# Kernel optimization log

Measured on AMD Instinct MI355X. Metric: run time of the kernel, lower is better.

The kernel has to match this reference:

```python
import jax, jax.numpy as jnp
import numpy as np
import math

D_MODEL = 1024
N_HEADS = 16
HEAD_DIM = D_MODEL // N_HEADS
RANK = 128
SCALE = 1.0 / math.sqrt(HEAD_DIM)


def lowrank(x, u, v, b):
    # y = (x @ u) @ v + b : d_model -> rank -> d_model
    return jnp.einsum('bsd,dr,re->bse', x, u, v) + b


def setup_inputs() -> dict:
    key = jax.random.key(0)
    ks = jax.random.split(key, 16)
    B, S = 2, 2048
    inp = {
        'q': jax.random.normal(ks[0], (B, S, D_MODEL), jnp.float32),
        'k': jax.random.normal(ks[1], (B, S, D_MODEL), jnp.float32),
        'v': jax.random.normal(ks[2], (B, S, D_MODEL), jnp.float32),
        'mask': jnp.ones((B, S), jnp.int32),
    }
    i = 3
    for name in ('q', 'k', 'v', 'out'):
        inp[f'{name}_u'] = jax.random.normal(ks[i], (D_MODEL, RANK), jnp.float32) * 0.02
        inp[f'{name}_v'] = jax.random.normal(ks[i + 1], (RANK, D_MODEL), jnp.float32) * 0.02
        inp[f'{name}_b'] = jnp.zeros((D_MODEL,), jnp.float32)
        i += 2
    return inp


def reference(q, k, v, mask, q_u, q_v, q_b, k_u, k_v, k_b, v_u, v_v, v_b, out_u, out_v, out_b):
    B, S, _ = q.shape
    qh = lowrank(q, q_u, q_v, q_b).reshape(B, S, N_HEADS, HEAD_DIM)
    kh = lowrank(k, k_u, k_v, k_b).reshape(B, S, N_HEADS, HEAD_DIM)
    vh = lowrank(v, v_u, v_v, v_b).reshape(B, S, N_HEADS, HEAD_DIM)
    # scores: [B, H, Sq, Sk]
    scores = jnp.einsum('bqhd,bkhd->bhqk', qh, kh) * SCALE
    scores = jnp.where(mask[:, None, None, :] == 0, -1e9, scores)
    attn = jax.nn.softmax(scores, axis=-1)
    ctx = jnp.einsum('bhqk,bkhd->bqhd', attn, vh).reshape(B, S, D_MODEL)
    return lowrank(ctx, out_u, out_v, out_b)
```

## Files before the change

### kernel.cpp

```cpp
#include <hip/hip_runtime.h>
#include <hip/hip_bf16.h>
#include <stdint.h>

#define DEVI __device__ __forceinline__

typedef __attribute__((ext_vector_type(8))) __bf16 bf16x8;
typedef __attribute__((ext_vector_type(4))) float f32x4;
typedef __attribute__((ext_vector_type(4))) unsigned short us4;

DEVI unsigned short f2bf(float x) {
  union { __bf16 b; unsigned short s; } u;
  u.b = (__bf16)x;
  return u.s;
}

DEVI f32x4 mfma16(bf16x8 a, bf16x8 b, f32x4 c) {
  return __builtin_amdgcn_mfma_f32_16x16x32_bf16(a, b, c, 0, 0, 0);
}

DEVI bf16x8 ld_frag(const unsigned short* tile, int row, int ld, int kbase, int lane) {
  const unsigned short* p = tile + row * ld + kbase + ((lane >> 4) << 2);
  union { bf16x8 f; us4 h[2]; } u;
  u.h[0] = *(const us4*)p;
  u.h[1] = *(const us4*)(p + 16);
  return u.f;
}

struct TP { const float* in[8]; unsigned short* out[8]; };

__global__ __launch_bounds__(256) void wtrans2(TP p) {
  const int z = blockIdx.y;
  const int R = (z & 1) ? 128 : 1024;
  const int C = (z & 1) ? 1024 : 128;
  __shared__ unsigned short T[32][33];
  const int tilesC = C >> 5;
  const int tr0 = (blockIdx.x / tilesC) << 5;
  const int tc0 = (blockIdx.x % tilesC) << 5;
  const int tx = threadIdx.x & 31, ty = threadIdx.x >> 5;
  #pragma unroll
  for (int j = 0; j < 4; j++)
    T[ty + j * 8][tx] = f2bf(p.in[z][(size_t)(tr0 + ty + j * 8) * C + tc0 + tx]);
  __syncthreads();
  #pragma unroll
  for (int j = 0; j < 4; j++)
    p.out[z][(size_t)(tc0 + ty + j * 8) * R + tr0 + tx] = T[tx][ty + j * 8];
}

struct GP {
  const void* A[3];
  const unsigned short* WT[3];
  const float* bias[3];
  void* C[3];
  float oscale[3];
};

template<bool ABF16, bool OBF16, bool BIAS>
__global__ __launch_bounds__(256)
void gemm_k(GP p, int M, int N, int K) {
  __shared__ unsigned short As[128][36];
  __shared__ unsigned short Ws[64][36];
  const int tid = threadIdx.x, lane = tid & 63, wid = tid >> 6;
  const int z = blockIdx.z;
  const int m0 = blockIdx.x * 128, n0 = blockIdx.y * 64;
  const int wm = (wid >> 1) * 64, wn = (wid & 1) * 32;
  f32x4 acc[4][2] = {};

  const int arow = tid >> 1, aseg = (tid & 1) * 16;
  const int wrow = tid >> 2, wseg = (tid & 3) * 8;
  const float* Af = (const float*)p.A[z];
  const unsigned short* Ab = (const unsigned short*)p.A[z];
  const unsigned short* Wt = p.WT[z];

  for (int k0 = 0; k0 < K; k0 += 32) {
    __syncthreads();
    {
      union { uint4 u[2]; us4 h[4]; unsigned short s[16]; } t;
      if (ABF16) {
        const unsigned short* src = Ab + (size_t)(m0 + arow) * K + k0 + aseg;
        t.u[0] = *(const uint4*)src;
        t.u[1] = *(const uint4*)(src + 8);
      } else {
        const float* src = Af + (size_t)(m0 + arow) * K + k0 + aseg;
        #pragma unroll
        for (int j = 0; j < 16; j += 4) {
          float4 f = *(const float4*)(src + j);
          t.s[j] = f2bf(f.x); t.s[j + 1] = f2bf(f.y);
          t.s[j + 2] = f2bf(f.z); t.s[j + 3] = f2bf(f.w);
        }
      }
      us4* dst = (us4*)&As[arow][aseg];
      dst[0] = t.h[0]; dst[1] = t.h[1]; dst[2] = t.h[2]; dst[3] = t.h[3];
    }
    {
      union { uint4 u; us4 h[2]; } t;
      const unsigned short* src = Wt + (size_t)(n0 + wrow) * K + k0 + wseg;
      t.u = *(const uint4*)src;
      us4* dst = (us4*)&Ws[wrow][wseg];
      dst[0] = t.h[0]; dst[1] = t.h[1];
    }
    __syncthreads();

    bf16x8 af[4], wf[2];
    #pragma unroll
    for (int mi = 0; mi < 4; mi++)
      af[mi] = ld_frag(&As[0][0], wm + mi * 16 + (lane & 15), 36, 0, lane);
    #pragma unroll
    for (int ni = 0; ni < 2; ni++)
      wf[ni] = ld_frag(&Ws[0][0], wn + ni * 16 + (lane & 15), 36, 0, lane);
    #pragma unroll
    for (int mi = 0; mi < 4; mi++)
      #pragma unroll
      for (int ni = 0; ni < 2; ni++)
        acc[mi][ni] = mfma16(af[mi], wf[ni], acc[mi][ni]);
  }

  const float os = p.oscale[z];
  #pragma unroll
  for (int ni = 0; ni < 2; ni++) {
    const int col = n0 + wn + ni * 16 + (lane & 15);
    const float bv = BIAS ? p.bias[z][col] : 0.0f;
    #pragma unroll
    for (int mi = 0; mi < 4; mi++)
      #pragma unroll
      for (int r = 0; r < 4; r++) {
        const int row = m0 + wm + mi * 16 + ((lane >> 4) << 2) + r;
        float vv = (acc[mi][ni][r] + bv) * os;
        if (OBF16) ((unsigned short*)p.C[z])[(size_t)row * N + col] = f2bf(vv);
        else       ((float*)p.C[z])[(size_t)row * N + col] = vv;
      }
  }
}

__global__ __launch_bounds__(256)
void attn_k2(const unsigned short* __restrict__ qh, const unsigned short* __restrict__ kh,
             const unsigned short* __restrict__ vh, const int* __restrict__ mask,
             unsigned short* __restrict__ ctx) {
  const int S = 2048, DM = 1024;
  __shared__ unsigned short Ks[64][68];
  __shared__ unsigned short VTs[64][68];
  __shared__ alignas(16) float mkadd[64];
  const int tid = threadIdx.x, lane = tid & 63, w = tid >> 6;
  const int b = blockIdx.z, h = blockIdx.y, q0 = blockIdx.x * 128;
  const int qbase = q0 + w * 32;
  const int lg4 = (lane >> 4) << 2, l15 = lane & 15;

  bf16x8 qf[2][2];
  #pragma unroll
  for (int ni = 0; ni < 2; ni++)
    #pragma unroll
    for (int kk = 0; kk < 2; kk++) {
      const unsigned short* p = qh + (size_t)(b * S + qbase + ni * 16 + l15) * DM
                                + h * 64 + kk * 32 + lg4;
      union { bf16x8 f; us4 h4[2]; } u;
      u.h4[0] = *(const us4*)p;
      u.h4[1] = *(const us4*)(p + 16);
      qf[ni][kk] = u.f;
    }

  float mrow[2], lrow[2];
  f32x4 acc_o[4][2] = {};
  mrow[0] = mrow[1] = -1e30f;
  lrow[0] = lrow[1] = 0.f;

  const int srow = tid >> 2, sseg = (tid & 3) * 16;

  for (int kv0 = 0; kv0 < S; kv0 += 64) {
    __syncthreads();
    {
      union { uint4 u[2]; us4 h[4]; unsigned short s[16]; } tk, tv;
      const unsigned short* ksrc = kh + (size_t)(b * S + kv0 + srow) * DM + h * 64 + sseg;
      tk.u[0] = *(const uint4*)ksrc; tk.u[1] = *(const uint4*)(ksrc + 8);
      us4* kd = (us4*)&Ks[srow][sseg];
      kd[0] = tk.h[0]; kd[1] = tk.h[1]; kd[2] = tk.h[2]; kd[3] = tk.h[3];
      const unsigned short* vsrc = vh + (size_t)(b * S + kv0 + srow) * DM + h * 64 + sseg;
      tv.u[0] = *(const uint4*)vsrc; tv.u[1] = *(const uint4*)(vsrc + 8);
      #pragma unroll
      for (int j = 0; j < 16; j++) VTs[sseg + j][srow] = tv.s[j];
      if (tid < 64) mkadd[tid] = (mask[b * S + kv0 + tid] == 0) ? -1e9f : 0.0f;
    }
    __syncthreads();

    f32x4 sc[4][2];
    #pragma unroll
    for (int mi = 0; mi < 4; mi++) {
      bf16x8 kf0 = ld_frag(&Ks[0][0], mi * 16 + l15, 68, 0, lane);
      bf16x8 kf1 = ld_frag(&Ks[0][0], mi * 16 + l15, 68, 32, lane);
      #pragma unroll
      for (int ni = 0; ni < 2; ni++) {
        f32x4 zz = {0.f, 0.f, 0.f, 0.f};
        zz = mfma16(kf0, qf[ni][0], zz);
        zz = mfma16(kf1, qf[ni][1], zz);
        sc[mi][ni] = zz;
      }
    }
    #pragma unroll
    for (int mi = 0; mi < 4; mi++) {
      f32x4 mv = *(const f32x4*)&mkadd[mi * 16 + lg4];
      #pragma unroll
      for (int ni = 0; ni < 2; ni++) sc[mi][ni] += mv;
    }

    #pragma unroll
    for (int ni = 0; ni < 2; ni++) {
      float pm = sc[0][ni][0];
      #pragma unroll
      for (int mi = 0; mi < 4; mi++)
        #pragma unroll
        for (int r = 0; r < 4; r++) pm = fmaxf(pm, sc[mi][ni][r]);
      pm = fmaxf(pm, __shfl_xor(pm, 16));
      pm = fmaxf(pm, __shfl_xor(pm, 32));
      const float mnew = fmaxf(mrow[ni], pm);
      const float alpha = __expf(mrow[ni] - mnew);
      mrow[ni] = mnew;
      float rs = 0.f;
      #pragma unroll
      for (int mi = 0; mi < 4; mi++)
        #pragma unroll
        for (int r = 0; r < 4; r++) {
          float e = __expf(sc[mi][ni][r] - mnew);
          sc[mi][ni][r] = e;
          rs += e;
        }
      rs += __shfl_xor(rs, 16);
      rs += __shfl_xor(rs, 32);
      lrow[ni] = lrow[ni] * alpha + rs;
      #pragma unroll
      for (int mi = 0; mi < 4; mi++) acc_o[mi][ni] *= alpha;
    }

    bf16x8 pb[2][2];
    #pragma unroll
    for (int kc = 0; kc < 2; kc++)
      #pragma unroll
      for (int ni = 0; ni < 2; ni++) {
        bf16x8 f;
        #pragma unroll
        for (int e = 0; e < 8; e++)
          f[e] = (__bf16)sc[2 * kc + (e >> 2)][ni][e & 3];
        pb[kc][ni] = f;
      }

    #pragma unroll
    for (int kc = 0; kc < 2; kc++) {
      #pragma unroll
      for (int mi = 0; mi < 4; mi++) {
        bf16x8 va = ld_frag(&VTs[0][0], mi * 16 + l15, 68, kc * 32, lane);
        acc_o[mi][0] = mfma16(va, pb[kc][0], acc_o[mi][0]);
        acc_o[mi][1] = mfma16(va, pb[kc][1], acc_o[mi][1]);
      }
    }
  }

  #pragma unroll
  for (int ni = 0; ni < 2; ni++) {
    const float rinv = 1.0f / lrow[ni];
    const size_t rowoff = (size_t)(b * S + qbase + ni * 16 + l15) * DM + h * 64;
    #pragma unroll
    for (int mi = 0; mi < 4; mi++) {
      us4 o;
      #pragma unroll
      for (int r = 0; r < 4; r++) o[r] = f2bf(acc_o[mi][ni][r] * rinv);
      *(us4*)(ctx + rowoff + mi * 16 + lg4) = o;
    }
  }
}

extern "C" void kernel_launch(void* const* d_in, const int* in_sizes, int n_in,
                              void* d_out, int out_size, void* d_ws, size_t ws_size,
                              hipStream_t stream) {
  const float* q = (const float*)d_in[0];
  const float* k = (const float*)d_in[1];
  const float* v = (const float*)d_in[2];
  const int* mask = (const int*)d_in[3];
  const float* wu[4] = {(const float*)d_in[4], (const float*)d_in[7],
                        (const float*)d_in[10], (const float*)d_in[13]};
  const float* wv[4] = {(const float*)d_in[5], (const float*)d_in[8],
                        (const float*)d_in[11], (const float*)d_in[14]};
  const float* wb[4] = {(const float*)d_in[6], (const float*)d_in[9],
                        (const float*)d_in[12], (const float*)d_in[15]};

  char* ws = (char*)d_ws;
  unsigned short* WT  = (unsigned short*)ws;
  unsigned short* T0  = (unsigned short*)(ws + 2097152);
  unsigned short* T1  = T0 + 524288;
  unsigned short* T2  = T1 + 524288;
  unsigned short* QH  = (unsigned short*)(ws + 2097152 + 3145728);
  unsigned short* KH  = QH + 4194304;
  unsigned short* VH  = KH + 4194304;
  unsigned short* CTX = VH + 4194304;

  TP tp;
  for (int i = 0; i < 4; i++) { tp.in[2 * i] = wu[i]; tp.in[2 * i + 1] = wv[i]; }
  for (int i = 0; i < 8; i++) tp.out[i] = WT + (size_t)i * 131072;
  wtrans2<<<dim3(128, 8), 256, 0, stream>>>(tp);

  const float SCALE = 0.125f;

  GP g1 = {};
  g1.A[0] = q; g1.A[1] = k; g1.A[2] = v;
  g1.WT[0] = tp.out[0]; g1.WT[1] = tp.out[2]; g1.WT[2] = tp.out[4];
  g1.C[0] = T0; g1.C[1] = T1; g1.C[2] = T2;
  g1.oscale[0] = g1.oscale[1] = g1.oscale[2] = 1.f;
  gemm_k<false, true, false><<<dim3(32, 2, 3), 256, 0, stream>>>(g1, 4096, 128, 1024);

  GP g2 = {};
  g2.A[0] = T0; g2.A[1] = T1; g2.A[2] = T2;
  g2.WT[0] = tp.out[1]; g2.WT[1] = tp.out[3]; g2.WT[2] = tp.out[5];
  g2.bias[0] = wb[0]; g2.bias[1] = wb[1]; g2.bias[2] = wb[2];
  g2.C[0] = QH; g2.C[1] = KH; g2.C[2] = VH;
  g2.oscale[0] = SCALE; g2.oscale[1] = 1.f; g2.oscale[2] = 1.f;
  gemm_k<true, true, true><<<dim3(32, 16, 3), 256, 0, stream>>>(g2, 4096, 1024, 128);

  attn_k2<<<dim3(16, 16, 2), 256, 0, stream>>>(QH, KH, VH, mask, CTX);

  GP g3 = {};
  g3.A[0] = CTX; g3.WT[0] = tp.out[6]; g3.C[0] = T0; g3.oscale[0] = 1.f;
  gemm_k<true, true, false><<<dim3(32, 2, 1), 256, 0, stream>>>(g3, 4096, 128, 1024);

  GP g4 = {};
  g4.A[0] = T0; g4.WT[0] = tp.out[7]; g4.bias[0] = wb[3];
  g4.C[0] = d_out; g4.oscale[0] = 1.f;
  gemm_k<true, false, true><<<dim3(32, 16, 1), 256, 0, stream>>>(g4, 4096, 1024, 128);
}
```

Before: 269.3 us.

## Fuse low-rank projection GEMM pairs and register-prefetch attention K/V tiles

Replaces the two-GEMM low-rank projections (x@U then @V) with one fused kernel per projection. The rank-128 intermediate now stays in shared memory instead of making a round trip through global memory, and the kernel launch count drops. Global loads for the next k-step are prefetched into registers in both the projection and the attention loops to overlap memory latency with MFMA work. In exchange, the fused kernel launches far fewer blocks (64 per projection), so GPU occupancy falls, and each block recomputes its full 1024-wide output serially.

Measured after the change: 259.6 us. 1.04x faster.

```diff
diff --git a/kernel.cpp b/kernel.cpp
--- a/kernel.cpp
+++ b/kernel.cpp
@@ -46,95 +46,149 @@
     p.out[z][(size_t)(tc0 + ty + j * 8) * R + tr0 + tx] = T[tx][ty + j * 8];
 }
 
-struct GP {
-  const void* A[3];
-  const unsigned short* WT[3];
+struct PJ {
+  const void* X[3];
+  const unsigned short* UT[3];
+  const unsigned short* VT[3];
   const float* bias[3];
-  void* C[3];
+  void* O[3];
   float oscale[3];
 };
 
-template<bool ABF16, bool OBF16, bool BIAS>
+template<bool ABF16, bool OF32>
 __global__ __launch_bounds__(256)
-void gemm_k(GP p, int M, int N, int K) {
-  __shared__ unsigned short As[128][36];
-  __shared__ unsigned short Ws[64][36];
-  const int tid = threadIdx.x, lane = tid & 63, wid = tid >> 6;
+void proj_fused(PJ p) {
+  __shared__ unsigned short SH[128 * 132 + 64 * 132];
+  unsigned short* Xs = SH;
+  unsigned short* Us = SH + 64 * 36;
+  unsigned short* Vs = SH;
+  unsigned short* Ts = SH + 128 * 132;
+
+  const int tid = threadIdx.x, lane = tid & 63, w = tid >> 6;
   const int z = blockIdx.z;
-  const int m0 = blockIdx.x * 128, n0 = blockIdx.y * 64;
-  const int wm = (wid >> 1) * 64, wn = (wid & 1) * 32;
-  f32x4 acc[4][2] = {};
-
-  const int arow = tid >> 1, aseg = (tid & 1) * 16;
-  const int wrow = tid >> 2, wseg = (tid & 3) * 8;
-  const float* Af = (const float*)p.A[z];
-  const unsigned short* Ab = (const unsigned short*)p.A[z];
-  const unsigned short* Wt = p.WT[z];
-
-  for (int k0 = 0; k0 < K; k0 += 32) {
-    __syncthreads();
-    {
-      union { uint4 u[2]; us4 h[4]; unsigned short s[16]; } t;
-      if (ABF16) {
-        const unsigned short* src = Ab + (size_t)(m0 + arow) * K + k0 + aseg;
-        t.u[0] = *(const uint4*)src;
-        t.u[1] = *(const uint4*)(src + 8);
-      } else {
-        const float* src = Af + (size_t)(m0 + arow) * K + k0 + aseg;
-        #pragma unroll
-        for (int j = 0; j < 16; j += 4) {
-          float4 f = *(const float4*)(src + j);
-          t.s[j] = f2bf(f.x); t.s[j + 1] = f2bf(f.y);
-          t.s[j + 2] = f2bf(f.z); t.s[j + 3] = f2bf(f.w);
-        }
-      }
-      us4* dst = (us4*)&As[arow][aseg];
-      dst[0] = t.h[0]; dst[1] = t.h[1]; dst[2] = t.h[2]; dst[3] = t.h[3];
-    }
+  const int m0 = blockIdx.x * 64;
+  const int lg4 = (lane >> 4) << 2, l15 = lane & 15;
+
+  const float* Xf = (const float*)p.X[z];
+  const unsigned short* Xb = (const unsigned short*)p.X[z];
+  const unsigned short* UT = p.UT[z];
+  const unsigned short* VT = p.VT[z];
+
+  const int xr = tid >> 2, xc = (tid & 3) * 8;
+  const int ur = tid >> 1, uc = (tid & 1) * 16;
+
+  float4 rx0, rx1; uint4 rxb;
+  uint4 ru0, ru1;
+  auto ldX = [&](int k0) {
+    if (ABF16) {
+      rxb = *(const uint4*)(Xb + (size_t)(m0 + xr) * 1024 + k0 + xc);
+    } else {
+      const float* s = Xf + (size_t)(m0 + xr) * 1024 + k0 + xc;
+      rx0 = *(const float4*)s; rx1 = *(const float4*)(s + 4);
+    }
+    const unsigned short* su = UT + (size_t)ur * 1024 + k0 + uc;
+    ru0 = *(const uint4*)su; ru1 = *(const uint4*)(su + 8);
+  };
+
+  f32x4 acc1[4][2] = {};
+  ldX(0);
+  for (int k0 = 0; k0 < 1024; k0 += 32) {
+    __syncthreads();
     {
       union { uint4 u; us4 h[2]; } t;
-      const unsigned short* src = Wt + (size_t)(n0 + wrow) * K + k0 + wseg;
-      t.u = *(const uint4*)src;
-      us4* dst = (us4*)&Ws[wrow][wseg];
-      dst[0] = t.h[0]; dst[1] = t.h[1];
-    }
+      us4* xd = (us4*)&Xs[xr * 36 + xc];
+      if (ABF16) {
+        t.u = rxb; xd[0] = t.h[0]; xd[1] = t.h[1];
+      } else {
+        us4 a, bq;
+        a[0] = f2bf(rx0.x); a[1] = f2bf(rx0.y); a[2] = f2bf(rx0.z); a[3] = f2bf(rx0.w);
+        bq[0] = f2bf(rx1.x); bq[1] = f2bf(rx1.y); bq[2] = f2bf(rx1.z); bq[3] = f2bf(rx1.w);
+        xd[0] = a; xd[1] = bq;
+      }
+      us4* udst = (us4*)&Us[ur * 36 + uc];
+      t.u = ru0; udst[0] = t.h[0]; udst[1] = t.h[1];
+      t.u = ru1; udst[2] = t.h[0]; udst[3] = t.h[1];
+    }
+    int kn = k0 + 32; if (kn > 992) kn = 992;
+    ldX(kn);
     __syncthreads();
 
     bf16x8 af[4], wf[2];
     #pragma unroll
     for (int mi = 0; mi < 4; mi++)
-      af[mi] = ld_frag(&As[0][0], wm + mi * 16 + (lane & 15), 36, 0, lane);
+      af[mi] = ld_frag(Xs, mi * 16 + l15, 36, 0, lane);
     #pragma unroll
     for (int ni = 0; ni < 2; ni++)
-      wf[ni] = ld_frag(&Ws[0][0], wn + ni * 16 + (lane & 15), 36, 0, lane);
+      wf[ni] = ld_frag(Us, w * 32 + ni * 16 + l15, 36, 0, lane);
     #pragma unroll
     for (int mi = 0; mi < 4; mi++)
       #pragma unroll
       for (int ni = 0; ni < 2; ni++)
-        acc[mi][ni] = mfma16(af[mi], wf[ni], acc[mi][ni]);
+        acc1[mi][ni] = mfma16(af[mi], wf[ni], acc1[mi][ni]);
   }
 
+  #pragma unroll
+  for (int mi = 0; mi < 4; mi++)
+    #pragma unroll
+    for (int ni = 0; ni < 2; ni++)
+      #pragma unroll
+      for (int r = 0; r < 4; r++)
+        Ts[(mi * 16 + lg4 + r) * 132 + w * 32 + ni * 16 + l15] = f2bf(acc1[mi][ni][r]);
+  __syncthreads();
+
+  bf16x8 af2[4][4];
+  #pragma unroll
+  for (int mi = 0; mi < 4; mi++)
+    #pragma unroll
+    for (int kc = 0; kc < 4; kc++)
+      af2[mi][kc] = ld_frag(Ts, mi * 16 + l15, 132, kc * 32, lane);
+
   const float os = p.oscale[z];
-  #pragma unroll
-  for (int ni = 0; ni < 2; ni++) {
-    const int col = n0 + wn + ni * 16 + (lane & 15);
-    const float bv = BIAS ? p.bias[z][col] : 0.0f;
-    #pragma unroll
-    for (int mi = 0; mi < 4; mi++)
-      #pragma unroll
-      for (int r = 0; r < 4; r++) {
-        const int row = m0 + wm + mi * 16 + ((lane >> 4) << 2) + r;
-        float vv = (acc[mi][ni][r] + bv) * os;
-        if (OBF16) ((unsigned short*)p.C[z])[(size_t)row * N + col] = f2bf(vv);
-        else       ((float*)p.C[z])[(size_t)row * N + col] = vv;
-      }
+  const int vr = tid >> 2, vc = (tid & 3) * 32;
+  for (int nc = 0; nc < 8; nc++) {
+    __syncthreads();
+    #pragma unroll
+    for (int pp = 0; pp < 2; pp++) {
+      const unsigned short* s = VT + (size_t)(nc * 128 + pp * 64 + vr) * 128 + vc;
+      uint4* d = (uint4*)&Vs[(pp * 64 + vr) * 132 + vc];
+      #pragma unroll
+      for (int j = 0; j < 4; j++) d[j] = *(const uint4*)(s + j * 8);
+    }
+    __syncthreads();
+
+    f32x4 acc2[4][2] = {};
+    #pragma unroll
+    for (int kc = 0; kc < 4; kc++) {
+      bf16x8 bf0 = ld_frag(Vs, w * 32 + 0 * 16 + l15, 132, kc * 32, lane);
+      bf16x8 bf1 = ld_frag(Vs, w * 32 + 1 * 16 + l15, 132, kc * 32, lane);
+      #pragma unroll
+      for (int mi = 0; mi < 4; mi++) {
+        acc2[mi][0] = mfma16(af2[mi][kc], bf0, acc2[mi][0]);
+        acc2[mi][1] = mfma16(af2[mi][kc], bf1, acc2[mi][1]);
+      }
+    }
+
+    #pragma unroll
+    for (int ni = 0; ni < 2; ni++) {
+      const int col = nc * 128 + w * 32 + ni * 16 + l15;
+      const float bv = p.bias[z][col];
+      #pragma unroll
+      for (int mi = 0; mi < 4; mi++)
+        #pragma unroll
+        for (int r = 0; r < 4; r++) {
+          const int row = m0 + mi * 16 + lg4 + r;
+          float vv = (acc2[mi][ni][r] + bv) * os;
+          if (OF32) ((float*)p.O[z])[(size_t)row * 1024 + col] = vv;
+          else ((unsigned short*)p.O[z])[(size_t)row * 1024 + col] = f2bf(vv);
+        }
+    }
   }
 }
 
 __global__ __launch_bounds__(256)
-void attn_k2(const unsigned short* __restrict__ qh, const unsigned short* __restrict__ kh,
-             const unsigned short* __restrict__ vh, const int* __restrict__ mask,
-             unsigned short* __restrict__ ctx) {
+void attn_k2p(const unsigned short* __restrict__ qh, const unsigned short* __restrict__ kh,
+              const unsigned short* __restrict__ vh, const int* __restrict__ mask,
+              unsigned short* __restrict__ ctx) {
   const int S = 2048, DM = 1024;
   __shared__ unsigned short Ks[64][68];
   __shared__ unsigned short VTs[64][68];
@@ -164,20 +218,30 @@
 
   const int srow = tid >> 2, sseg = (tid & 3) * 16;
 
+  uint4 rk0, rk1, rv0, rv1; int rmI = 1;
+  auto ldT = [&](int kv0) {
+    const unsigned short* ksrc = kh + (size_t)(b * S + kv0 + srow) * DM + h * 64 + sseg;
+    rk0 = *(const uint4*)ksrc; rk1 = *(const uint4*)(ksrc + 8);
+    const unsigned short* vsrc = vh + (size_t)(b * S + kv0 + srow) * DM + h * 64 + sseg;
+    rv0 = *(const uint4*)vsrc; rv1 = *(const uint4*)(vsrc + 8);
+    if (tid < 64) rmI = mask[b * S + kv0 + tid];
+  };
+  ldT(0);
+
   for (int kv0 = 0; kv0 < S; kv0 += 64) {
     __syncthreads();
     {
-      union { uint4 u[2]; us4 h[4]; unsigned short s[16]; } tk, tv;
-      const unsigned short* ksrc = kh + (size_t)(b * S + kv0 + srow) * DM + h * 64 + sseg;
-      tk.u[0] = *(const uint4*)ksrc; tk.u[1] = *(const uint4*)(ksrc + 8);
+      union { uint4 u[2]; unsigned short s[16]; us4 h[4]; } tk, tv;
+      tk.u[0] = rk0; tk.u[1] = rk1;
       us4* kd = (us4*)&Ks[srow][sseg];
       kd[0] = tk.h[0]; kd[1] = tk.h[1]; kd[2] = tk.h[2]; kd[3] = tk.h[3];
-      const unsigned short* vsrc = vh + (size_t)(b * S + kv0 + srow) * DM + h * 64 + sseg;
-      tv.u[0] = *(const uint4*)vsrc; tv.u[1] = *(const uint4*)(vsrc + 8);
+      tv.u[0] = rv0; tv.u[1] = rv1;
       #pragma unroll
       for (int j = 0; j < 16; j++) VTs[sseg + j][srow] = tv.s[j];
-      if (tid < 64) mkadd[tid] = (mask[b * S + kv0 + tid] == 0) ? -1e9f : 0.0f;
-    }
+      if (tid < 64) mkadd[tid] = (rmI == 0) ? -1e9f : 0.0f;
+    }
+    int nxt = kv0 + 64; if (nxt >= S) nxt = kv0;
+    ldT(nxt);
     __syncthreads();
 
     f32x4 sc[4][2];
@@ -281,10 +345,7 @@
 
   char* ws = (char*)d_ws;
   unsigned short* WT  = (unsigned short*)ws;
-  unsigned short* T0  = (unsigned short*)(ws + 2097152);
-  unsigned short* T1  = T0 + 524288;
-  unsigned short* T2  = T1 + 524288;
-  unsigned short* QH  = (unsigned short*)(ws + 2097152 + 3145728);
+  unsigned short* QH  = (unsigned short*)(ws + 2097152);
   unsigned short* KH  = QH + 4194304;
   unsigned short* VH  = KH + 4194304;
   unsigned short* CTX = VH + 4194304;
@@ -296,29 +357,23 @@
 
   const float SCALE = 0.125f;
 
-  GP g1 = {};
-  g1.A[0] = q; g1.A[1] = k; g1.A[2] = v;
-  g1.WT[0] = tp.out[0]; g1.WT[1] = tp.out[2]; g1.WT[2] = tp.out[4];
-  g1.C[0] = T0; g1.C[1] = T1; g1.C[2] = T2;
-  g1.oscale[0] = g1.oscale[1] = g1.oscale[2] = 1.f;
-  gemm_k<false, true, false><<<dim3(32, 2, 3), 256, 0, stream>>>(g1, 4096, 128, 1024);
-
-  GP g2 = {};
-  g2.A[0] = T0; g2.A[1] = T1; g2.A[2] = T2;
-  g2.WT[0] = tp.out[1]; g2.WT[1] = tp.out[3]; g2.WT[2] = tp.out[5];
-  g2.bias[0] = wb[0]; g2.bias[1] = wb[1]; g2.bias[2] = wb[2];
-  g2.C[0] = QH; g2.C[1] = KH; g2.C[2] = VH;
-  g2.oscale[0] = SCALE; g2.oscale[1] = 1.f; g2.oscale[2] = 1.f;
-  gemm_k<true, true, true><<<dim3(32, 16, 3), 256, 0, stream>>>(g2, 4096, 1024, 128);
-
-  attn_k2<<<dim3(16, 16, 2), 256, 0, stream>>>(QH, KH, VH, mask, CTX);
-
-  GP g3 = {};
-  g3.A[0] = CTX; g3.WT[0] = tp.out[6]; g3.C[0] = T0; g3.oscale[0] = 1.f;
-  gemm_k<true, true, false><<<dim3(32, 2, 1), 256, 0, stream>>>(g3, 4096, 128, 1024);
-
-  GP g4 = {};
-  g4.A[0] = T0; g4.WT[0] = tp.out[7]; g4.bias[0] = wb[3];
-  g4.C[0] = d_out; g4.oscale[0] = 1.f;
-  gemm_k<true, false, true><<<dim3(32, 16, 1), 256, 0, stream>>>(g4, 4096, 1024, 128);
-}
+  PJ pq = {};
+  pq.X[0] = q; pq.X[1] = k; pq.X[2] = v;
+  pq.UT[0] = tp.out[0]; pq.UT[1] = tp.out[2]; pq.UT[2] = tp.out[4];
+  pq.VT[0] = tp.out[1]; pq.VT[1] = tp.out[3]; pq.VT[2] = tp.out[5];
+  pq.bias[0] = wb[0]; pq.bias[1] = wb[1]; pq.bias[2] = wb[2];
+  pq.O[0] = QH; pq.O[1] = KH; pq.O[2] = VH;
+  pq.oscale[0] = SCALE; pq.oscale[1] = 1.f; pq.oscale[2] = 1.f;
+  proj_fused<false, false><<<dim3(64, 1, 3), 256, 0, stream>>>(pq);
+
+  attn_k2p<<<dim3(16, 16, 2), 256, 0, stream>>>(QH, KH, VH, mask, CTX);
+
+  PJ po = {};
+  po.X[0] = CTX;
+  po.UT[0] = tp.out[6];
+  po.VT[0] = tp.out[7];
+  po.bias[0] = wb[3];
+  po.O[0] = d_out;
+  po.oscale[0] = 1.f;
+  proj_fused<true, true><<<dim3(64, 1, 1), 256, 0, stream>>>(po);
+}
```
